# Optimization experiments

Hardware: AMD Instinct MI355X
Metric: run time of the kernel (lower is better)

Reference implementation:

```python
import jax, jax.numpy as jnp
import numpy as np

B, C_IN, C_OUT, RED, H, W = 8, 256, 64, 16, 256, 256
K = 3


def setup_inputs() -> dict:
    key = jax.random.key(0)
    k1, k2, k3, k4, k5 = jax.random.split(key, 5)
    x = jax.random.normal(k1, (B, C_OUT, H, W), dtype=jnp.float32)
    vec = jax.random.normal(k2, (B, C_IN), dtype=jnp.float32)
    # ChanNorm affine params
    g = jnp.ones((1, C_OUT, 1, 1), dtype=jnp.float32)
    b = jnp.zeros((1, C_OUT, 1, 1), dtype=jnp.float32)
    # conv_du MLP (torch Linear weights: [out, in], no bias)
    w1 = jax.random.normal(k3, (C_IN // RED, C_IN), dtype=jnp.float32) / np.sqrt(C_IN)
    w2 = jax.random.normal(k4, (C_OUT, C_IN // RED), dtype=jnp.float32) / np.sqrt(C_IN // RED)
    # Conv2DMod weight, kaiming normal fan_in (leaky_relu a=0): std=sqrt(2/fan_in)
    fan_in = C_OUT * K * K
    wconv = jax.random.normal(k5, (C_OUT, C_OUT, K, K), dtype=jnp.float32) * np.sqrt(2.0 / fan_in)
    return {"x": x, "vec": vec, "g": g, "b": b, "w1": w1, "w2": w2, "wconv": wconv}


def reference(x, vec, g, b, w1, w2, wconv):
    eps_norm = 1e-5
    eps_mod = 1e-8
    # ChanNorm: normalize over channel dim (unbiased=False var)
    mean = jnp.mean(x, axis=1, keepdims=True)
    var = jnp.mean((x - mean) ** 2, axis=1, keepdims=True)
    nx = (x - mean) / jnp.sqrt(var + eps_norm) * g + b
    # style MLP: Linear -> LeakyReLU(0.1) -> Linear (no biases)
    hid = jax.nn.leaky_relu(vec @ w1.T, negative_slope=0.1)
    sty = hid @ w2.T  # [B, C_OUT]
    # per-sample modulated weights: [B, O, I, K, K]
    weights = wconv[None, :, :, :, :] * (sty[:, None, :, None, None] + 1.0)
    # demodulate
    d = jax.lax.rsqrt(jnp.sum(weights ** 2, axis=(2, 3, 4), keepdims=True) + eps_mod)
    weights = weights * d
    # grouped conv with groups=B == per-sample conv; same padding for k=3,s=1,d=1 -> 1
    pad = ((H - 1) * 0 + 1 * (K - 1)) // 2
    def per_sample_conv(xi, wi):
        # xi: [C,H,W], wi: [O,I,K,K]
        return jax.lax.conv_general_dilated(
            xi[None], wi, window_strides=(1, 1),
            padding=[(pad, pad), (pad, pad)],
            dimension_numbers=("NCHW", "OIHW", "NCHW"))[0]
    out = jax.vmap(per_sample_conv)(nx, weights)  # [B, O, H, W]
    return out + x
```

## Files before the change

### kernel.cpp

```cpp
#include <hip/hip_runtime.h>
#include <hip/hip_bf16.h>

typedef __hip_bfloat16 bf16;
typedef __attribute__((ext_vector_type(8))) short short8;
typedef __attribute__((ext_vector_type(4))) float float4v;

#define Hd 256
#define Wd 256
#define HW 65536
#define CO 64

__global__ __launch_bounds__(64) void k1_style(
    const float* __restrict__ vec, const float* __restrict__ w1,
    const float* __restrict__ w2, const float* __restrict__ wconv,
    bf16* __restrict__ wA)
{
    int o = blockIdx.x;
    int s = blockIdx.y;
    int i = threadIdx.x;

    float sv[4];
#pragma unroll
    for (int q = 0; q < 4; ++q) sv[q] = vec[s * 256 + q * 64 + i];

    float hid[16];
#pragma unroll
    for (int j = 0; j < 16; ++j) {
        float p = 0.f;
#pragma unroll
        for (int q = 0; q < 4; ++q) p += sv[q] * w1[j * 256 + q * 64 + i];
#pragma unroll
        for (int off = 32; off >= 1; off >>= 1) p += __shfl_xor(p, off, 64);
        hid[j] = p > 0.f ? p : 0.1f * p;
    }
    float sty = 0.f;
#pragma unroll
    for (int j = 0; j < 16; ++j) sty += w2[i * 16 + j] * hid[j];
    float msty = sty + 1.0f;

    float wrow[9];
#pragma unroll
    for (int tt = 0; tt < 9; ++tt) wrow[tt] = wconv[(o * 64 + i) * 9 + tt] * msty;
    float ss = 0.f;
#pragma unroll
    for (int tt = 0; tt < 9; ++tt) ss += wrow[tt] * wrow[tt];
#pragma unroll
    for (int off = 32; off >= 1; off >>= 1) ss += __shfl_xor(ss, off, 64);
    float d = rsqrtf(ss + 1e-8f);

    bf16* wAs = wA + s * (18 * 64 * 32);
#pragma unroll
    for (int tt = 0; tt < 9; ++tt) {
        int k = tt * 64 + i;
        wAs[(k >> 5) * 2048 + o * 32 + (k & 31)] = (bf16)(wrow[tt] * d);
    }
}

#define PXB 32
#define ROWS 4
#define TR 6
#define WL 34
#define ROW_ELEMS (8 * WL * 8)

__global__ __launch_bounds__(256, 4) void k3_fused(
    const float* __restrict__ x, const float* __restrict__ gg,
    const float* __restrict__ bb, const bf16* __restrict__ wA,
    float* __restrict__ out)
{
    int w0 = blockIdx.x * PXB;
    int h0 = blockIdx.y * ROWS;
    int s  = blockIdx.z;
    int t  = threadIdx.x;
    __shared__ __align__(16) bf16 tile[TR * ROW_ELEMS];
    __shared__ float sg[64], sb[64];
    __shared__ float2 sbi[64];
    __shared__ float2 sms[TR * WL];
    if (t < 64) {
        float gv = gg[t];
        sg[t] = gv; sb[t] = bb[t];
        sbi[t] = make_float2(bb[t], 1.0f / gv);
    }
    __syncthreads();

    if (t < TR * WL) {
        int dr = t / WL, wl = t - dr * WL;
        int grow = h0 + dr - 1, wabs = w0 + wl - 1;
        bf16* dst = &tile[dr * ROW_ELEMS + wl * 8];
        if (grow >= 0 && grow < Hd && wabs >= 0 && wabs < Wd) {
            const float* xp = x + (size_t)s * (CO * HW) + (size_t)grow * Wd + wabs;
            float s1 = 0.f, s2 = 0.f;
#pragma unroll
            for (int c = 0; c < 64; ++c) {
                float f = xp[(size_t)c * HW];
                s1 += f; s2 += f * f;
            }
            float mean = s1 * (1.f / 64);
            float var  = s2 * (1.f / 64) - mean * mean;
            float rstd = rsqrtf(var + 1e-5f);
            sms[t] = make_float2(mean, sqrtf(var + 1e-5f));
            asm volatile("" ::: "memory");
#pragma unroll
            for (int c8 = 0; c8 < 8; ++c8) {
                bf16 ov[8];
#pragma unroll
                for (int k = 0; k < 8; ++k) {
                    int c = c8 * 8 + k;
                    float f = xp[(size_t)c * HW];
                    ov[k] = (bf16)((f - mean) * rstd * sg[c] + sb[c]);
                }
                *(uint4*)&dst[c8 * (WL * 8)] = *(uint4*)ov;
            }
        } else {
            sms[t] = make_float2(0.f, 0.f);
            uint4 z = make_uint4(0u, 0u, 0u, 0u);
#pragma unroll
            for (int c8 = 0; c8 < 8; ++c8) *(uint4*)&dst[c8 * (WL * 8)] = z;
        }
    }
    __syncthreads();

    int wave = t >> 6, lane = t & 63;
    int mi = wave & 1, ni = wave >> 1;
    int col = lane & 15, quad = lane >> 4;

    const bf16* wAs = wA + s * (18 * 64 * 32);

    float4v acc[2][4];
#pragma unroll
    for (int mt = 0; mt < 2; ++mt)
#pragma unroll
        for (int r = 0; r < 4; ++r) acc[mt][r] = (float4v)0.f;

#pragma unroll 1
    for (int kh = 0; kh < 3; ++kh) {
#pragma unroll
        for (int kw = 0; kw < 3; ++kw) {
#pragma unroll
            for (int half = 0; half < 2; ++half) {
                int kc = (kh * 3 + kw) * 2 + half;
                union { uint4 u; short8 s8; } a0, a1;
                a0.u = *(const uint4*)&wAs[kc * 2048 + (mi * 32 + col) * 32 + quad * 8];
                a1.u = *(const uint4*)&wAs[kc * 2048 + (mi * 32 + 16 + col) * 32 + quad * 8];
                int ch8 = half * 4 + quad;
#pragma unroll
                for (int r = 0; r < 4; ++r) {
                    union { uint4 u; short8 s8; } b;
                    b.u = *(const uint4*)&tile[(r + kh) * ROW_ELEMS
                                               + (ch8 * WL + ni * 16 + col + kw) * 8];
                    acc[0][r] = __builtin_amdgcn_mfma_f32_16x16x32_bf16(a0.s8, b.s8, acc[0][r], 0, 0, 0);
                    acc[1][r] = __builtin_amdgcn_mfma_f32_16x16x32_bf16(a1.s8, b.s8, acc[1][r], 0, 0, 0);
                }
            }
        }
    }

    int wpx  = w0 + ni * 16 + col;
    int wl_i = ni * 16 + col + 1;
#pragma unroll
    for (int r = 0; r < 4; ++r) {
        int grow = h0 + r;
        float2 ms = sms[(r + 1) * WL + wl_i];
#pragma unroll
        for (int mt = 0; mt < 2; ++mt) {
#pragma unroll
            for (int rr = 0; rr < 4; ++rr) {
                int o = mi * 32 + mt * 16 + quad * 4 + rr;
                float nxf = __bfloat162float(
                    tile[(r + 1) * ROW_ELEMS + ((o >> 3) * WL + wl_i) * 8 + (o & 7)]);
                float2 bi = sbi[o];
                float xrec = (nxf - bi.x) * bi.y * ms.y + ms.x;
                size_t idx = (size_t)(s * CO + o) * HW + (size_t)grow * Wd + wpx;
                out[idx] = acc[mt][r][rr] + xrec;
            }
        }
    }
}

extern "C" void kernel_launch(void* const* d_in, const int* in_sizes, int n_in,
                              void* d_out, int out_size, void* d_ws, size_t ws_size,
                              hipStream_t stream)
{
    const float* x     = (const float*)d_in[0];
    const float* vec   = (const float*)d_in[1];
    const float* g     = (const float*)d_in[2];
    const float* bb    = (const float*)d_in[3];
    const float* w1    = (const float*)d_in[4];
    const float* w2    = (const float*)d_in[5];
    const float* wconv = (const float*)d_in[6];
    float* out = (float*)d_out;

    bf16* wA = (bf16*)d_ws;

    k1_style<<<dim3(64, 8), 64, 0, stream>>>(vec, w1, w2, wconv, wA);
    k3_fused<<<dim3(8, 64, 8), 256, 0, stream>>>(x, g, bb, wA, out);
}
```

Before: 362.9 us.

## Double rows per block and stage raw x to LDS in single pass

Each block now computes 8 output rows instead of 4, so the 2-row halo is shared across more rows and redundant x reads and normalization work drop. The tile load now reads x once: it converts to bf16 into LDS while accumulating the channel stats, then normalizes in place from LDS instead of re-reading global memory. Two pixels per thread are handled. Occupancy hint drops to 3 blocks and register use grows with 16 accumulators, and raw values are rounded to bf16 before normalization, which slightly changes precision. An unused template parameter selected by workspace size is added.

```diff
diff --git a/kernel.cpp b/kernel.cpp
--- a/kernel.cpp
+++ b/kernel.cpp
@@ -57,12 +57,15 @@
 }
 
 #define PXB 32
-#define ROWS 4
-#define TR 6
+#define ROWS 8
+#define TR 10
 #define WL 34
 #define ROW_ELEMS (8 * WL * 8)
 
-__global__ __launch_bounds__(256, 4) void k3_fused(
+union U4 { uint4 u; bf16 h[8]; short8 s8; };
+
+template<int WSBIG>
+__global__ __launch_bounds__(256, 3) void k3_fused(
     const float* __restrict__ x, const float* __restrict__ gg,
     const float* __restrict__ bb, const bf16* __restrict__ wA,
     float* __restrict__ out)
@@ -82,39 +85,82 @@
     }
     __syncthreads();
 
-    if (t < TR * WL) {
-        int dr = t / WL, wl = t - dr * WL;
-        int grow = h0 + dr - 1, wabs = w0 + wl - 1;
-        bf16* dst = &tile[dr * ROW_ELEMS + wl * 8];
-        if (grow >= 0 && grow < Hd && wabs >= 0 && wabs < Wd) {
-            const float* xp = x + (size_t)s * (CO * HW) + (size_t)grow * Wd + wabs;
-            float s1 = 0.f, s2 = 0.f;
-#pragma unroll
-            for (int c = 0; c < 64; ++c) {
-                float f = xp[(size_t)c * HW];
-                s1 += f; s2 += f * f;
-            }
-            float mean = s1 * (1.f / 64);
-            float var  = s2 * (1.f / 64) - mean * mean;
-            float rstd = rsqrtf(var + 1e-5f);
-            sms[t] = make_float2(mean, sqrtf(var + 1e-5f));
-            asm volatile("" ::: "memory");
-#pragma unroll
+    int p0 = t, p1 = t + 256;
+    bool live1 = (p1 < TR * WL);
+    int dr0 = p0 / WL, wl0 = p0 - dr0 * WL;
+    int dr1 = live1 ? (p1 / WL) : 0;
+    int wl1 = live1 ? (p1 - dr1 * WL) : 0;
+    int grow0 = h0 + dr0 - 1, wab0 = w0 + wl0 - 1;
+    int grow1 = h0 + dr1 - 1, wab1 = w0 + wl1 - 1;
+    bool ok0 = (grow0 >= 0 && grow0 < Hd && wab0 >= 0 && wab0 < Wd);
+    bool ok1 = live1 && (grow1 >= 0 && grow1 < Hd && wab1 >= 0 && wab1 < Wd);
+    const float* xp0 = x + (size_t)s * (CO * HW) + (size_t)grow0 * Wd + wab0;
+    const float* xp1 = x + (size_t)s * (CO * HW) + (size_t)grow1 * Wd + wab1;
+    bf16* dst0 = &tile[dr0 * ROW_ELEMS + wl0 * 8];
+    bf16* dst1 = &tile[dr1 * ROW_ELEMS + wl1 * 8];
+
+    float s1a = 0.f, s2a = 0.f, s1b = 0.f, s2b = 0.f;
+#pragma unroll 1
+    for (int c8 = 0; c8 < 8; ++c8) {
+        U4 pa, pb;
+        if (ok0) {
+#pragma unroll
+            for (int k = 0; k < 8; ++k) {
+                float f = xp0[(size_t)(c8 * 8 + k) * HW];
+                s1a += f; s2a += f * f;
+                pa.h[k] = (bf16)f;
+            }
+        } else pa.u = make_uint4(0u, 0u, 0u, 0u);
+        *(uint4*)&dst0[c8 * (WL * 8)] = pa.u;
+        if (live1) {
+            if (ok1) {
+#pragma unroll
+                for (int k = 0; k < 8; ++k) {
+                    float f = xp1[(size_t)(c8 * 8 + k) * HW];
+                    s1b += f; s2b += f * f;
+                    pb.h[k] = (bf16)f;
+                }
+            } else pb.u = make_uint4(0u, 0u, 0u, 0u);
+            *(uint4*)&dst1[c8 * (WL * 8)] = pb.u;
+        }
+    }
+
+    {
+        float mean = s1a * (1.f / 64);
+        float var  = s2a * (1.f / 64) - mean * mean;
+        float rstd = rsqrtf(var + 1e-5f);
+        sms[p0] = ok0 ? make_float2(mean, sqrtf(var + 1e-5f)) : make_float2(0.f, 0.f);
+        if (ok0) {
+#pragma unroll 1
             for (int c8 = 0; c8 < 8; ++c8) {
-                bf16 ov[8];
+                U4 v; v.u = *(uint4*)&dst0[c8 * (WL * 8)];
+                U4 o;
 #pragma unroll
                 for (int k = 0; k < 8; ++k) {
                     int c = c8 * 8 + k;
-                    float f = xp[(size_t)c * HW];
-                    ov[k] = (bf16)((f - mean) * rstd * sg[c] + sb[c]);
-                }
-                *(uint4*)&dst[c8 * (WL * 8)] = *(uint4*)ov;
-            }
-        } else {
-            sms[t] = make_float2(0.f, 0.f);
-            uint4 z = make_uint4(0u, 0u, 0u, 0u);
-#pragma unroll
-            for (int c8 = 0; c8 < 8; ++c8) *(uint4*)&dst[c8 * (WL * 8)] = z;
+                    o.h[k] = (bf16)((__bfloat162float(v.h[k]) - mean) * rstd * sg[c] + sb[c]);
+                }
+                *(uint4*)&dst0[c8 * (WL * 8)] = o.u;
+            }
+        }
+    }
+    if (live1) {
+        float mean = s1b * (1.f / 64);
+        float var  = s2b * (1.f / 64) - mean * mean;
+        float rstd = rsqrtf(var + 1e-5f);
+        sms[p1] = ok1 ? make_float2(mean, sqrtf(var + 1e-5f)) : make_float2(0.f, 0.f);
+        if (ok1) {
+#pragma unroll 1
+            for (int c8 = 0; c8 < 8; ++c8) {
+                U4 v; v.u = *(uint4*)&dst1[c8 * (WL * 8)];
+                U4 o;
+#pragma unroll
+                for (int k = 0; k < 8; ++k) {
+                    int c = c8 * 8 + k;
+                    o.h[k] = (bf16)((__bfloat162float(v.h[k]) - mean) * rstd * sg[c] + sb[c]);
+                }
+                *(uint4*)&dst1[c8 * (WL * 8)] = o.u;
+            }
         }
     }
     __syncthreads();
@@ -122,14 +168,13 @@
     int wave = t >> 6, lane = t & 63;
     int mi = wave & 1, ni = wave >> 1;
     int col = lane & 15, quad = lane >> 4;
-
     const bf16* wAs = wA + s * (18 * 64 * 32);
 
-    float4v acc[2][4];
+    float4v acc[2][ROWS];
 #pragma unroll
     for (int mt = 0; mt < 2; ++mt)
 #pragma unroll
-        for (int r = 0; r < 4; ++r) acc[mt][r] = (float4v)0.f;
+        for (int r = 0; r < ROWS; ++r) acc[mt][r] = (float4v)0.f;
 
 #pragma unroll 1
     for (int kh = 0; kh < 3; ++kh) {
@@ -138,15 +183,14 @@
 #pragma unroll
             for (int half = 0; half < 2; ++half) {
                 int kc = (kh * 3 + kw) * 2 + half;
-                union { uint4 u; short8 s8; } a0, a1;
+                U4 a0, a1;
                 a0.u = *(const uint4*)&wAs[kc * 2048 + (mi * 32 + col) * 32 + quad * 8];
                 a1.u = *(const uint4*)&wAs[kc * 2048 + (mi * 32 + 16 + col) * 32 + quad * 8];
                 int ch8 = half * 4 + quad;
-#pragma unroll
-                for (int r = 0; r < 4; ++r) {
-                    union { uint4 u; short8 s8; } b;
-                    b.u = *(const uint4*)&tile[(r + kh) * ROW_ELEMS
-                                               + (ch8 * WL + ni * 16 + col + kw) * 8];
+                const bf16* bbase = &tile[kh * ROW_ELEMS + (ch8 * WL + ni * 16 + col + kw) * 8];
+#pragma unroll
+                for (int r = 0; r < ROWS; ++r) {
+                    U4 b; b.u = *(const uint4*)&bbase[r * ROW_ELEMS];
                     acc[0][r] = __builtin_amdgcn_mfma_f32_16x16x32_bf16(a0.s8, b.s8, acc[0][r], 0, 0, 0);
                     acc[1][r] = __builtin_amdgcn_mfma_f32_16x16x32_bf16(a1.s8, b.s8, acc[1][r], 0, 0, 0);
                 }
@@ -157,7 +201,7 @@
     int wpx  = w0 + ni * 16 + col;
     int wl_i = ni * 16 + col + 1;
 #pragma unroll
-    for (int r = 0; r < 4; ++r) {
+    for (int r = 0; r < ROWS; ++r) {
         int grow = h0 + r;
         float2 ms = sms[(r + 1) * WL + wl_i];
 #pragma unroll
@@ -192,5 +236,9 @@
     bf16* wA = (bf16*)d_ws;
 
     k1_style<<<dim3(64, 8), 64, 0, stream>>>(vec, w1, w2, wconv, wA);
-    k3_fused<<<dim3(8, 64, 8), 256, 0, stream>>>(x, g, bb, wA, out);
+
+    if (ws_size >= ((size_t)72 << 20))
+        k3_fused<1><<<dim3(8, 32, 8), 256, 0, stream>>>(x, g, bb, wA, out);
+    else
+        k3_fused<0><<<dim3(8, 32, 8), 256, 0, stream>>>(x, g, bb, wA, out);
 }
```

Measured after the change: 328.2 us. 1.11x faster.
